# Kernel optimization log

Hardware: AMD Instinct MI355X
Metric: run time of the kernel (lower is better)

The kernel has to match this reference:

```python
import jax, jax.numpy as jnp
import numpy as np

B, N, D = 8, 4096, 1024
NC, NU = 8, 32            # core / universal experts (num_experts=16, occ_factor=1/4)
E = NC + NU               # 40 total experts
S = 2                     # slots per expert
HC, HU = 4 * D, D         # core hidden = 4*dim, occ hidden = 4*occ_factor*dim = dim
L2_EPS = 1e-6
LN_EPS = 1e-5


def l2norm(x):
    n = jnp.sqrt(jnp.sum(x * x, axis=-1, keepdims=True))
    return x * (1.0 / (n + L2_EPS))


def layernorm(x, g, b):
    mu = jnp.mean(x, axis=-1, keepdims=True)
    var = jnp.mean((x - mu) ** 2, axis=-1, keepdims=True)
    return (x - mu) / jnp.sqrt(var + LN_EPS) * g + b


def entmax15(z):
    # exact 1.5-entmax over last axis (sorted algorithm, Peters et al. 2019)
    z = z / 2.0
    z = z - jnp.max(z, axis=-1, keepdims=True)
    zs = -jnp.sort(-z, axis=-1)                      # descending
    K = z.shape[-1]
    k = jnp.arange(1, K + 1, dtype=z.dtype)
    mean = jnp.cumsum(zs, axis=-1) / k
    meansq = jnp.cumsum(zs * zs, axis=-1) / k
    ss = k * (meansq - mean * mean)
    delta = jnp.maximum((1.0 - ss) / k, 1e-12)
    tau = mean - jnp.sqrt(delta)
    support = jnp.sum((tau <= zs).astype(jnp.int32), axis=-1, keepdims=True)
    tau_star = jnp.take_along_axis(tau, support - 1, axis=-1)
    return jnp.maximum(z - tau_star, 0.0) ** 2


def setup_inputs() -> dict:
    key = jax.random.key(0)
    ks = jax.random.split(key, 8)
    return {
        "x": jax.random.normal(ks[0], (B, N, D), jnp.float32),
        "attn_weight": jax.random.uniform(ks[1], (B, 128), jnp.float32),
        "phi": jax.random.normal(ks[2], (E, S, D), jnp.float32) * 0.02,
        "key_gamma": jnp.ones((D,), jnp.float32),
        "key_beta": jnp.zeros((D,), jnp.float32),
        "query_gamma": jnp.ones((D,), jnp.float32),
        "query_beta": jnp.zeros((D,), jnp.float32),
        "ln_gamma": jnp.ones((D,), jnp.float32),
        "ln_beta": jnp.zeros((D,), jnp.float32),
        "scale0": jnp.asarray(0.5, jnp.float32),
        "scale1": jnp.asarray(0.5, jnp.float32),
        "core_w1": jax.random.normal(ks[3], (NC, D, HC), jnp.float32) * (D ** -0.5),
        "core_b1": jnp.zeros((NC, HC), jnp.float32),
        "core_w2": jax.random.normal(ks[4], (NC, HC, D), jnp.float32) * (HC ** -0.5),
        "core_b2": jnp.zeros((NC, D), jnp.float32),
        "occ_w1": jax.random.normal(ks[5], (NU, D, HU), jnp.float32) * (D ** -0.5),
        "occ_b1": jnp.zeros((NU, HU), jnp.float32),
        "occ_w2": jax.random.normal(ks[6], (NU, HU, D), jnp.float32) * (HU ** -0.5),
        "occ_b2": jnp.zeros((NU, D), jnp.float32),
    }


def _expert_mlp(s, w1, b1, w2, b2):
    # s: [b, e, s, d]; per-expert 2-layer MLP with exact GELU
    h = jax.nn.gelu(jnp.einsum('besd,edh->besh', s, w1) + b1[None, :, None, :], approximate=False)
    return jnp.einsum('besh,ehd->besd', h, w2) + b2[None, :, None, :]


def reference(x, attn_weight, phi, key_gamma, key_beta, query_gamma, query_beta,
              ln_gamma, ln_beta, scale0, scale1,
              core_w1, core_b1, core_w2, core_b2,
              occ_w1, occ_b1, occ_w2, occ_b2):
    # keys: OffsetScale then l2norm
    k = l2norm(x * key_gamma + key_beta)
    # queries: OffsetScale -> LayerNorm -> l2norm on phi
    q = layernorm(phi * query_gamma + query_beta, ln_gamma, ln_beta)
    q = l2norm(q)
    logits = jnp.einsum('bnd,esd->bnes', k, q)                      # [B,N,E,S]
    core_mask = (jnp.arange(E) < NC)[None, None, :, None]
    adjusted = jnp.where(core_mask, logits, jnp.asarray(-10000.0, logits.dtype))
    dispatch = jax.nn.softmax(adjusted / scale0, axis=2)            # softmax over experts
    combine = entmax15((adjusted / scale1).reshape(B, N, E * S))    # [B,N,E*S]
    slots = jnp.einsum('bnd,bnes->besd', x, dispatch)               # [B,E,S,D]
    core_out = _expert_mlp(slots[:, :NC], core_w1, core_b1, core_w2, core_b2)
    occ_out = _expert_mlp(slots[:, NC:], occ_w1, occ_b1, occ_w2, occ_b2)
    out = jnp.concatenate([core_out, occ_out], axis=1).reshape(B, E * S, D)
    return jnp.einsum('bsd,bns->bnd', out, combine)                 # [B,N,D]
```

## Files before the change

kernel.cpp:

```cpp
#include <hip/hip_runtime.h>
#include <hip/hip_bf16.h>

#define B_ 8
#define N_ 4096
#define D_ 1024

__global__ __launch_bounds__(64) void k_prep(
    const float* __restrict__ phi, const float* __restrict__ qg, const float* __restrict__ qb,
    const float* __restrict__ lng, const float* __restrict__ lnb,
    const float* __restrict__ kg, const float* __restrict__ kb,
    float* __restrict__ qk, float* __restrict__ cj, float* __restrict__ wbuf)
{
    int r = blockIdx.x;
    int lane = threadIdx.x;
    if (r == 16) {
        float cacc = 0.f;
#pragma unroll
        for (int c = 0; c < 16; ++c) {
            int i = c * 64 + lane;
            float g = kg[i], b = kb[i];
            wbuf[i] = g * g;
            wbuf[1024 + i] = 2.0f * g * b;
            cacc += b * b;
        }
#pragma unroll
        for (int m = 32; m; m >>= 1) cacc += __shfl_xor(cacc, m);
        if (lane == 0) wbuf[2048] = cacc;
        return;
    }
    const float* pr = phi + (size_t)r * D_;
    float v[16];
    float s1 = 0.f;
#pragma unroll
    for (int c = 0; c < 16; ++c) {
        int i = c * 64 + lane;
        v[c] = pr[i] * qg[i] + qb[i];
        s1 += v[c];
    }
#pragma unroll
    for (int m = 32; m; m >>= 1) s1 += __shfl_xor(s1, m);
    float mu = s1 * (1.0f / D_);
    float s2 = 0.f;
#pragma unroll
    for (int c = 0; c < 16; ++c) { float dd = v[c] - mu; s2 += dd * dd; }
#pragma unroll
    for (int m = 32; m; m >>= 1) s2 += __shfl_xor(s2, m);
    float var = s2 * (1.0f / D_);
    float inv = 1.0f / sqrtf(var + 1e-5f);
    float u[16];
    float s3 = 0.f;
#pragma unroll
    for (int c = 0; c < 16; ++c) {
        int i = c * 64 + lane;
        u[c] = (v[c] - mu) * inv * lng[i] + lnb[i];
        s3 += u[c] * u[c];
    }
#pragma unroll
    for (int m = 32; m; m >>= 1) s3 += __shfl_xor(s3, m);
    float rn = 1.0f / (sqrtf(s3) + 1e-6f);
    float cacc = 0.f;
#pragma unroll
    for (int c = 0; c < 16; ++c) {
        int i = c * 64 + lane;
        float qv = u[c] * rn;
        qk[(size_t)r * D_ + i] = qv * kg[i];
        cacc += qv * kb[i];
    }
#pragma unroll
    for (int m = 32; m; m >>= 1) cacc += __shfl_xor(cacc, m);
    if (lane == 0) cj[r] = cacc;
}

__global__ __launch_bounds__(256) void k_logits(
    const float* __restrict__ x, const float* __restrict__ qk,
    const float* __restrict__ wbuf, float* __restrict__ lgbuf)
{
    __shared__ float xs[2][32 * 68];
    __shared__ float qs[2][16 * 64];
    __shared__ float wsd[2][128];

    int tid = threadIdx.x;
    int tok0 = blockIdx.x * 32;
    int tok = tid & 31, gg = tid >> 5;

    float acc[17];
#pragma unroll
    for (int v = 0; v < 17; ++v) acc[v] = 0.f;

    float4 rx0, rx1, rq;
    float rw = 0.f;
    int r0 = tid >> 4, c40 = tid & 15;
    int r1 = 16 + r0;

    auto STAGE = [&](int dc) {
        rx0 = *(const float4*)(x + (size_t)(tok0 + r0) * D_ + dc * 64 + c40 * 4);
        rx1 = *(const float4*)(x + (size_t)(tok0 + r1) * D_ + dc * 64 + c40 * 4);
        rq  = *(const float4*)(qk + (size_t)(tid >> 4) * D_ + dc * 64 + (tid & 15) * 4);
        if (tid < 128) rw = wbuf[(size_t)(tid >> 6) * 1024 + dc * 64 + (tid & 63)];
    };
    auto WRITE = [&](int buf) {
        *(float4*)(&xs[buf][r0 * 68 + c40 * 4]) = rx0;
        *(float4*)(&xs[buf][r1 * 68 + c40 * 4]) = rx1;
        ((float4*)qs[buf])[tid] = rq;
        if (tid < 128) wsd[buf][tid] = rw;
    };
    auto COMPUTE = [&](int buf) {
        const float* xp = &xs[buf][tok * 68 + gg * 8];
        const float* qp = &qs[buf][gg * 8];
        const float* wp = &wsd[buf][gg * 8];
#pragma unroll
        for (int dl4 = 0; dl4 < 2; ++dl4) {
            float4 xv  = *(const float4*)(xp + dl4 * 4);
            float4 w2v = *(const float4*)(wp + dl4 * 4);
            float4 w1v = *(const float4*)(wp + 64 + dl4 * 4);
            acc[16] += (w2v.x * xv.x + w1v.x) * xv.x + (w2v.y * xv.y + w1v.y) * xv.y
                     + (w2v.z * xv.z + w1v.z) * xv.z + (w2v.w * xv.w + w1v.w) * xv.w;
#pragma unroll
            for (int j = 0; j < 16; ++j) {
                float4 q4 = *(const float4*)(qp + j * 64 + dl4 * 4);
                acc[j] += xv.x * q4.x + xv.y * q4.y + xv.z * q4.z + xv.w * q4.w;
            }
        }
    };

    STAGE(0);
    WRITE(0);
    int cur = 0;
#pragma unroll 1
    for (int dc = 0; dc < 16; ++dc) {
        if (dc < 15) STAGE(dc + 1);
        __syncthreads();
        COMPUTE(cur);
        if (dc < 15) WRITE(cur ^ 1);
        cur ^= 1;
    }
    __syncthreads();

    float* red = &xs[0][0];
#pragma unroll
    for (int v = 0; v < 17; ++v) red[(tok * 17 + v) * 8 + gg] = acc[v];
    __syncthreads();

#pragma unroll
    for (int it = 0; it < 3; ++it) {
        int idx = tid + it * 256;
        if (idx < 544) {
            float4 p0 = *(const float4*)(red + idx * 8);
            float4 p1 = *(const float4*)(red + idx * 8 + 4);
            float sum = ((p0.x + p0.y) + (p0.z + p0.w)) + ((p1.x + p1.y) + (p1.z + p1.w));
            int t = idx / 17, v = idx - t * 17;
            lgbuf[(size_t)(tok0 + t) * 20 + v] = sum;
        }
    }
}

__global__ __launch_bounds__(64) void k_epi(
    const float* __restrict__ lgbuf, const float* __restrict__ cj,
    const float* __restrict__ wbuf,
    const float* __restrict__ s0p, const float* __restrict__ s1p,
    float* __restrict__ combine, float* __restrict__ dispatch)
{
    int tok = blockIdx.x * 64 + threadIdx.x;
    const float* lp = lgbuf + (size_t)tok * 20;
    float s[17];
    float4 q0 = *(const float4*)(lp + 0);
    float4 q1 = *(const float4*)(lp + 4);
    float4 q2 = *(const float4*)(lp + 8);
    float4 q3 = *(const float4*)(lp + 12);
    s[0] = q0.x; s[1] = q0.y; s[2] = q0.z; s[3] = q0.w;
    s[4] = q1.x; s[5] = q1.y; s[6] = q1.z; s[7] = q1.w;
    s[8] = q2.x; s[9] = q2.y; s[10] = q2.z; s[11] = q2.w;
    s[12] = q3.x; s[13] = q3.y; s[14] = q3.z; s[15] = q3.w;
    s[16] = lp[16];

    float ss = s[16] + wbuf[2048];
    float rn = 1.0f / (sqrtf(ss) + 1e-6f);
    float inv0 = 1.0f / s0p[0];
    float inv1h = 0.5f / s1p[0];
    float lg[16];
#pragma unroll
    for (int j = 0; j < 16; ++j) lg[j] = (s[j] + cj[j]) * rn;

    float dsp[16];
#pragma unroll
    for (int sl = 0; sl < 2; ++sl) {
        float a[8], m = -1e30f;
#pragma unroll
        for (int ee = 0; ee < 8; ++ee) { a[ee] = lg[2 * ee + sl] * inv0; m = fmaxf(m, a[ee]); }
        float den = 0.f;
#pragma unroll
        for (int ee = 0; ee < 8; ++ee) { a[ee] = expf(a[ee] - m); den += a[ee]; }
        float r = 1.0f / den;
#pragma unroll
        for (int ee = 0; ee < 8; ++ee) dsp[2 * ee + sl] = a[ee] * r;
    }

    float z[16], zmax = -1e30f;
#pragma unroll
    for (int j = 0; j < 16; ++j) { z[j] = lg[j] * inv1h; zmax = fmaxf(zmax, z[j]); }
#pragma unroll
    for (int j = 0; j < 16; ++j) z[j] -= zmax;
    float zsr[16];
#pragma unroll
    for (int j = 0; j < 16; ++j) zsr[j] = z[j];
#pragma unroll
    for (int rr = 0; rr < 16; ++rr) {
#pragma unroll
        for (int jj = (rr & 1); jj + 1 < 16; jj += 2) {
            float aa = zsr[jj], bb = zsr[jj + 1];
            zsr[jj] = fmaxf(aa, bb);
            zsr[jj + 1] = fminf(aa, bb);
        }
    }
    float cs = 0.f, css = 0.f, tau_star = 0.f;
#pragma unroll
    for (int kk = 1; kk <= 16; ++kk) {
        cs += zsr[kk - 1];
        css += zsr[kk - 1] * zsr[kk - 1];
        float fk = (float)kk;
        float mean = cs / fk, msq = css / fk;
        float ssv = fk * (msq - mean * mean);
        float delta = fmaxf((1.0f - ssv) / fk, 1e-12f);
        float tau = mean - sqrtf(delta);
        tau_star = (tau <= zsr[kk - 1]) ? tau : tau_star;
    }
    float4* cw = (float4*)(combine + (size_t)tok * 16);
    float4* dw = (float4*)(dispatch + (size_t)tok * 16);
#pragma unroll
    for (int q4i = 0; q4i < 4; ++q4i) {
        float4 cv, dv;
        float t0 = fmaxf(z[q4i * 4 + 0] - tau_star, 0.f);
        float t1 = fmaxf(z[q4i * 4 + 1] - tau_star, 0.f);
        float t2 = fmaxf(z[q4i * 4 + 2] - tau_star, 0.f);
        float t3 = fmaxf(z[q4i * 4 + 3] - tau_star, 0.f);
        cv.x = t0 * t0; cv.y = t1 * t1; cv.z = t2 * t2; cv.w = t3 * t3;
        dv.x = dsp[q4i * 4 + 0]; dv.y = dsp[q4i * 4 + 1];
        dv.z = dsp[q4i * 4 + 2]; dv.w = dsp[q4i * 4 + 3];
        cw[q4i] = cv;
        dw[q4i] = dv;
    }
}

__global__ __launch_bounds__(256) void k_slots_partial(
    const float* __restrict__ x, const float* __restrict__ dispatch,
    float* __restrict__ partial)
{
    __shared__ float sm[2048];
    int nc = blockIdx.x, dc = blockIdx.y, b = blockIdx.z;
    int tid = threadIdx.x;
    int n0 = nc * 128;
    int d0 = dc * 512 + tid * 2;
    const float4* src = (const float4*)(dispatch + ((size_t)b * N_ + n0) * 16);
    ((float4*)sm)[tid * 2] = src[tid * 2];
    ((float4*)sm)[tid * 2 + 1] = src[tid * 2 + 1];
    __syncthreads();

    const float* xp = x + ((size_t)b * N_ + n0) * D_ + d0;
    float2 acc[16];
#pragma unroll
    for (int j = 0; j < 16; ++j) { acc[j].x = 0.f; acc[j].y = 0.f; }
#pragma unroll 4
    for (int n = 0; n < 128; ++n) {
        float2 xv = *(const float2*)(xp + (size_t)n * D_);
        const float4* q4 = (const float4*)(sm + n * 16);
        float4 s0 = q4[0], s1 = q4[1], s2 = q4[2], s3 = q4[3];
        acc[0].x  += s0.x * xv.x; acc[0].y  += s0.x * xv.y;
        acc[1].x  += s0.y * xv.x; acc[1].y  += s0.y * xv.y;
        acc[2].x  += s0.z * xv.x; acc[2].y  += s0.z * xv.y;
        acc[3].x  += s0.w * xv.x; acc[3].y  += s0.w * xv.y;
        acc[4].x  += s1.x * xv.x; acc[4].y  += s1.x * xv.y;
        acc[5].x  += s1.y * xv.x; acc[5].y  += s1.y * xv.y;
        acc[6].x  += s1.z * xv.x; acc[6].y  += s1.z * xv.y;
        acc[7].x  += s1.w * xv.x; acc[7].y  += s1.w * xv.y;
        acc[8].x  += s2.x * xv.x; acc[8].y  += s2.x * xv.y;
        acc[9].x  += s2.y * xv.x; acc[9].y  += s2.y * xv.y;
        acc[10].x += s2.z * xv.x; acc[10].y += s2.z * xv.y;
        acc[11].x += s2.w * xv.x; acc[11].y += s2.w * xv.y;
        acc[12].x += s3.x * xv.x; acc[12].y += s3.x * xv.y;
        acc[13].x += s3.y * xv.x; acc[13].y += s3.y * xv.y;
        acc[14].x += s3.z * xv.x; acc[14].y += s3.z * xv.y;
        acc[15].x += s3.w * xv.x; acc[15].y += s3.w * xv.y;
    }
    float* op = partial + (((size_t)b * 32 + nc) * 16) * 1024 + d0;
#pragma unroll
    for (int j = 0; j < 16; ++j)
        *(float2*)(op + (size_t)j * 1024) = acc[j];
}

__global__ __launch_bounds__(256) void k_slots_reduce(
    const float* __restrict__ partial, float* __restrict__ slotsT)
{
    int idx = blockIdx.x * 256 + threadIdx.x;
    int t = idx & 15;
    int k = (idx >> 4) & 1023;
    int e = idx >> 14;
    int b = t >> 1, s = t & 1;
    int j = e * 2 + s;
    const float* p = partial + ((size_t)(b * 32) * 16 + j) * 1024 + k;
    float sum = 0.f;
#pragma unroll
    for (int nc = 0; nc < 32; ++nc) sum += p[(size_t)nc * 16384];
    slotsT[idx] = sum;
}

__global__ __launch_bounds__(256) void k_mlp1(
    const float* __restrict__ w1, const float* __restrict__ slotsT,
    float* __restrict__ p1)
{
    __shared__ float sm[2048];
    int cc = blockIdx.x, ks = blockIdx.y, e = blockIdx.z;
    int tid = threadIdx.x;
    int k0 = ks * 128;
    int col = cc * 512 + tid * 2;
    const float4* src = (const float4*)(slotsT + ((size_t)e * 1024 + k0) * 16);
    ((float4*)sm)[tid * 2] = src[tid * 2];
    ((float4*)sm)[tid * 2 + 1] = src[tid * 2 + 1];
    __syncthreads();

    const float* wp = w1 + (size_t)e * 1024 * 4096 + (size_t)k0 * 4096 + col;
    float2 acc[16];
#pragma unroll
    for (int t = 0; t < 16; ++t) { acc[t].x = 0.f; acc[t].y = 0.f; }
#pragma unroll 4
    for (int kk = 0; kk < 128; ++kk) {
        float2 w = *(const float2*)(wp + (size_t)kk * 4096);
        const float4* q4 = (const float4*)(sm + kk * 16);
        float4 s0 = q4[0], s1 = q4[1], s2 = q4[2], s3 = q4[3];
        acc[0].x  += s0.x * w.x; acc[0].y  += s0.x * w.y;
        acc[1].x  += s0.y * w.x; acc[1].y  += s0.y * w.y;
        acc[2].x  += s0.z * w.x; acc[2].y  += s0.z * w.y;
        acc[3].x  += s0.w * w.x; acc[3].y  += s0.w * w.y;
        acc[4].x  += s1.x * w.x; acc[4].y  += s1.x * w.y;
        acc[5].x  += s1.y * w.x; acc[5].y  += s1.y * w.y;
        acc[6].x  += s1.z * w.x; acc[6].y  += s1.z * w.y;
        acc[7].x  += s1.w * w.x; acc[7].y  += s1.w * w.y;
        acc[8].x  += s2.x * w.x; acc[8].y  += s2.x * w.y;
        acc[9].x  += s2.y * w.x; acc[9].y  += s2.y * w.y;
        acc[10].x += s2.z * w.x; acc[10].y += s2.z * w.y;
        acc[11].x += s2.w * w.x; acc[11].y += s2.w * w.y;
        acc[12].x += s3.x * w.x; acc[12].y += s3.x * w.y;
        acc[13].x += s3.y * w.x; acc[13].y += s3.y * w.y;
        acc[14].x += s3.z * w.x; acc[14].y += s3.z * w.y;
        acc[15].x += s3.w * w.x; acc[15].y += s3.w * w.y;
    }
    float* op = p1 + (((size_t)ks * 8 + e) * 4096 + col) * 16;
#pragma unroll
    for (int q = 0; q < 4; ++q) {
        float4 a, b;
        a.x = acc[q * 4 + 0].x; a.y = acc[q * 4 + 1].x; a.z = acc[q * 4 + 2].x; a.w = acc[q * 4 + 3].x;
        b.x = acc[q * 4 + 0].y; b.y = acc[q * 4 + 1].y; b.z = acc[q * 4 + 2].y; b.w = acc[q * 4 + 3].y;
        *(float4*)(op + q * 4) = a;
        *(float4*)(op + 16 + q * 4) = b;
    }
}

__global__ __launch_bounds__(256) void k_red1(
    const float* __restrict__ p1, const float* __restrict__ b1,
    float* __restrict__ hT)
{
    int idx = blockIdx.x * 256 + threadIdx.x;
    int q = idx & 3, col = (idx >> 2) & 4095, e = idx >> 14;
    const float* p = p1 + ((size_t)e * 4096 + col) * 16 + q * 4;
    float4 s; s.x = 0.f; s.y = 0.f; s.z = 0.f; s.w = 0.f;
#pragma unroll
    for (int ks = 0; ks < 8; ++ks) {
        float4 v = *(const float4*)(p + (size_t)ks * 524288);
        s.x += v.x; s.y += v.y; s.z += v.z; s.w += v.w;
    }
    float bb = b1[(size_t)e * 4096 + col];
    s.x += bb; s.y += bb; s.z += bb; s.w += bb;
    s.x = 0.5f * s.x * (1.0f + erff(s.x * 0.70710678118654752f));
    s.y = 0.5f * s.y * (1.0f + erff(s.y * 0.70710678118654752f));
    s.z = 0.5f * s.z * (1.0f + erff(s.z * 0.70710678118654752f));
    s.w = 0.5f * s.w * (1.0f + erff(s.w * 0.70710678118654752f));
    *(float4*)(hT + ((size_t)e * 4096 + col) * 16 + q * 4) = s;
}

__global__ __launch_bounds__(256) void k_mlp2(
    const float* __restrict__ w2, const float* __restrict__ hT,
    float* __restrict__ p2)
{
    __shared__ float sm[2048];
    int cc = blockIdx.x, ks = blockIdx.y, e = blockIdx.z;
    int tid = threadIdx.x;
    int k0 = ks * 128;
    int col = cc * 512 + tid * 2;
    const float4* src = (const float4*)(hT + ((size_t)e * 4096 + k0) * 16);
    ((float4*)sm)[tid * 2] = src[tid * 2];
    ((float4*)sm)[tid * 2 + 1] = src[tid * 2 + 1];
    __syncthreads();

    const float* wp = w2 + (size_t)e * 4096 * 1024 + (size_t)k0 * 1024 + col;
    float2 acc[16];
#pragma unroll
    for (int t = 0; t < 16; ++t) { acc[t].x = 0.f; acc[t].y = 0.f; }
#pragma unroll 4
    for (int kk = 0; kk < 128; ++kk) {
        float2 w = *(const float2*)(wp + (size_t)kk * 1024);
        const float4* q4 = (const float4*)(sm + kk * 16);
        float4 s0 = q4[0], s1 = q4[1], s2 = q4[2], s3 = q4[3];
        acc[0].x  += s0.x * w.x; acc[0].y  += s0.x * w.y;
        acc[1].x  += s0.y * w.x; acc[1].y  += s0.y * w.y;
        acc[2].x  += s0.z * w.x; acc[2].y  += s0.z * w.y;
        acc[3].x  += s0.w * w.x; acc[3].y  += s0.w * w.y;
        acc[4].x  += s1.x * w.x; acc[4].y  += s1.x * w.y;
        acc[5].x  += s1.y * w.x; acc[5].y  += s1.y * w.y;
        acc[6].x  += s1.z * w.x; acc[6].y  += s1.z * w.y;
        acc[7].x  += s1.w * w.x; acc[7].y  += s1.w * w.y;
        acc[8].x  += s2.x * w.x; acc[8].y  += s2.x * w.y;
        acc[9].x  += s2.y * w.x; acc[9].y  += s2.y * w.y;
        acc[10].x += s2.z * w.x; acc[10].y += s2.z * w.y;
        acc[11].x += s2.w * w.x; acc[11].y += s2.w * w.y;
        acc[12].x += s3.x * w.x; acc[12].y += s3.x * w.y;
        acc[13].x += s3.y * w.x; acc[13].y += s3.y * w.y;
        acc[14].x += s3.z * w.x; acc[14].y += s3.z * w.y;
        acc[15].x += s3.w * w.x; acc[15].y += s3.w * w.y;
    }
    float* op = p2 + (((size_t)ks * 8 + e) * 1024 + col) * 16;
#pragma unroll
    for (int q = 0; q < 4; ++q) {
        float4 a, b;
        a.x = acc[q * 4 + 0].x; a.y = acc[q * 4 + 1].x; a.z = acc[q * 4 + 2].x; a.w = acc[q * 4 + 3].x;
        b.x = acc[q * 4 + 0].y; b.y = acc[q * 4 + 1].y; b.z = acc[q * 4 + 2].y; b.w = acc[q * 4 + 3].y;
        *(float4*)(op + q * 4) = a;
        *(float4*)(op + 16 + q * 4) = b;
    }
}

__global__ __launch_bounds__(256) void k_red2(
    const float* __restrict__ p2, const float* __restrict__ b2,
    float* __restrict__ co)
{
    int idx = blockIdx.x * 256 + threadIdx.x;
    if (idx >= 8192) return;
    int d = idx & 1023, e = idx >> 10;
    const float* p = p2 + ((size_t)e * 1024 + d) * 16;
    float4 a0, a1, a2, a3;
    a0.x=a0.y=a0.z=a0.w=0.f; a1.x=a1.y=a1.z=a1.w=0.f;
    a2.x=a2.y=a2.z=a2.w=0.f; a3.x=a3.y=a3.z=a3.w=0.f;
#pragma unroll
    for (int ks = 0; ks < 32; ++ks) {
        const float4* v = (const float4*)(p + (size_t)ks * 131072);
        float4 v0 = v[0], v1 = v[1], v2 = v[2], v3 = v[3];
        a0.x += v0.x; a0.y += v0.y; a0.z += v0.z; a0.w += v0.w;
        a1.x += v1.x; a1.y += v1.y; a1.z += v1.z; a1.w += v1.w;
        a2.x += v2.x; a2.y += v2.y; a2.z += v2.z; a2.w += v2.w;
        a3.x += v3.x; a3.y += v3.y; a3.z += v3.z; a3.w += v3.w;
    }
    float bb = b2[(size_t)e * 1024 + d];
    float vv[16] = { a0.x, a0.y, a0.z, a0.w, a1.x, a1.y, a1.z, a1.w,
                     a2.x, a2.y, a2.z, a2.w, a3.x, a3.y, a3.z, a3.w };
#pragma unroll
    for (int t = 0; t < 16; ++t) {
        int b = t >> 1, s = t & 1;
        co[((size_t)b * 16 + e * 2 + s) * 1024 + d] = vv[t] + bb;
    }
}

__global__ __launch_bounds__(256) void k_out(
    const float* __restrict__ co, const float* __restrict__ combine,
    float* __restrict__ out)
{
    int b = blockIdx.y, tile = blockIdx.x;
    int tid = threadIdx.x;
    float4 cv[16];
#pragma unroll
    for (int j = 0; j < 16; ++j)
        cv[j] = ((const float4*)(co + ((size_t)b * 16 + j) * 1024))[tid];
    const float* cb = combine + ((size_t)b * N_ + tile * 64) * 16;
    float4* ob = (float4*)(out + ((size_t)b * N_ + tile * 64) * 1024) + tid;
    for (int it = 0; it < 64; ++it) {
        const float* cm = cb + it * 16;
        float4 acc; acc.x = 0.f; acc.y = 0.f; acc.z = 0.f; acc.w = 0.f;
#pragma unroll
        for (int j = 0; j < 16; ++j) {
            float wj = cm[j];
            acc.x += wj * cv[j].x; acc.y += wj * cv[j].y;
            acc.z += wj * cv[j].z; acc.w += wj * cv[j].w;
        }
        ob[(size_t)it * 256] = acc;
    }
}

extern "C" void kernel_launch(void* const* d_in, const int* in_sizes, int n_in,
                              void* d_out, int out_size, void* d_ws, size_t ws_size,
                              hipStream_t stream)
{
    const float* x   = (const float*)d_in[0];
    const float* phi = (const float*)d_in[2];
    const float* kg  = (const float*)d_in[3];
    const float* kb  = (const float*)d_in[4];
    const float* qg  = (const float*)d_in[5];
    const float* qb  = (const float*)d_in[6];
    const float* lng = (const float*)d_in[7];
    const float* lnb = (const float*)d_in[8];
    const float* s0  = (const float*)d_in[9];
    const float* s1  = (const float*)d_in[10];
    const float* w1  = (const float*)d_in[11];
    const float* b1  = (const float*)d_in[12];
    const float* w2  = (const float*)d_in[13];
    const float* b2  = (const float*)d_in[14];

    float* out = (float*)d_out;
    float* ws  = (float*)d_ws;

    float* qk       = ws;
    float* cj       = qk + 16384;
    float* wbuf     = cj + 16;
    float* combine  = wbuf + 2064;
    float* dispatch = combine + 524288;
    float* slotsT   = dispatch + 524288;
    float* hT       = slotsT + 131072;
    float* co       = hT + 524288;
    float* arena    = co + 131072;
    float* lgbuf    = arena;
    float* spart    = arena;
    float* p1       = arena;
    float* p2       = arena;

    k_prep         <<<dim3(17),         dim3(64),  0, stream>>>(phi, qg, qb, lng, lnb, kg, kb, qk, cj, wbuf);
    k_logits       <<<dim3(1024),       dim3(256), 0, stream>>>(x, qk, wbuf, lgbuf);
    k_epi          <<<dim3(512),        dim3(64),  0, stream>>>(lgbuf, cj, wbuf, s0, s1, combine, dispatch);
    k_slots_partial<<<dim3(32, 2, 8),   dim3(256), 0, stream>>>(x, dispatch, spart);
    k_slots_reduce <<<dim3(512),        dim3(256), 0, stream>>>(spart, slotsT);
    k_mlp1         <<<dim3(8, 8, 8),    dim3(256), 0, stream>>>(w1, slotsT, p1);
    k_red1         <<<dim3(512),        dim3(256), 0, stream>>>(p1, b1, hT);
    k_mlp2         <<<dim3(2, 32, 8),   dim3(256), 0, stream>>>(w2, hT, p2);
    k_red2         <<<dim3(32),         dim3(256), 0, stream>>>(p2, b2, co);
    k_out          <<<dim3(64, 8),      dim3(256), 0, stream>>>(co, combine, out);
}
```

Measured before the change: 246.6 us.

## Retile logits, slots and expert MLP kernels for wider per-thread work

Each k_logits block now computes 64 tokens instead of 32, so the staged q vectors are reused across two token sets. The slots and both MLP GEMV-style kernels switch from float2 to float4 columns per thread and use shorter K chunks, which gives more split-K partials and different grids. The slots and second-layer reductions are restructured to match, and k_out stages the combine weights in shared memory. The aim is better register reuse and wider memory accesses, at the cost of more partial-sum traffic and higher register pressure.

```diff
diff --git a/kernel.cpp b/kernel.cpp
--- a/kernel.cpp
+++ b/kernel.cpp
@@ -75,50 +75,56 @@
     const float* __restrict__ x, const float* __restrict__ qk,
     const float* __restrict__ wbuf, float* __restrict__ lgbuf)
 {
-    __shared__ float xs[2][32 * 68];
+    __shared__ float xs[2][64 * 68];
     __shared__ float qs[2][16 * 64];
     __shared__ float wsd[2][128];
 
     int tid = threadIdx.x;
-    int tok0 = blockIdx.x * 32;
-    int tok = tid & 31, gg = tid >> 5;
-
-    float acc[17];
-#pragma unroll
-    for (int v = 0; v < 17; ++v) acc[v] = 0.f;
-
-    float4 rx0, rx1, rq;
+    int tok0 = blockIdx.x * 64;
+    int tok32 = tid & 31, gg = tid >> 5;
+    int sr = tid >> 4, sc = tid & 15;
+
+    float accA[17], accB[17];
+#pragma unroll
+    for (int v = 0; v < 17; ++v) { accA[v] = 0.f; accB[v] = 0.f; }
+
+    float4 rx[4], rq;
     float rw = 0.f;
-    int r0 = tid >> 4, c40 = tid & 15;
-    int r1 = 16 + r0;
 
     auto STAGE = [&](int dc) {
-        rx0 = *(const float4*)(x + (size_t)(tok0 + r0) * D_ + dc * 64 + c40 * 4);
-        rx1 = *(const float4*)(x + (size_t)(tok0 + r1) * D_ + dc * 64 + c40 * 4);
-        rq  = *(const float4*)(qk + (size_t)(tid >> 4) * D_ + dc * 64 + (tid & 15) * 4);
+#pragma unroll
+        for (int i = 0; i < 4; ++i)
+            rx[i] = *(const float4*)(x + (size_t)(tok0 + sr + 16 * i) * D_ + dc * 64 + sc * 4);
+        rq = *(const float4*)(qk + (size_t)sr * D_ + dc * 64 + sc * 4);
         if (tid < 128) rw = wbuf[(size_t)(tid >> 6) * 1024 + dc * 64 + (tid & 63)];
     };
     auto WRITE = [&](int buf) {
-        *(float4*)(&xs[buf][r0 * 68 + c40 * 4]) = rx0;
-        *(float4*)(&xs[buf][r1 * 68 + c40 * 4]) = rx1;
+#pragma unroll
+        for (int i = 0; i < 4; ++i)
+            *(float4*)(&xs[buf][(sr + 16 * i) * 68 + sc * 4]) = rx[i];
         ((float4*)qs[buf])[tid] = rq;
         if (tid < 128) wsd[buf][tid] = rw;
     };
     auto COMPUTE = [&](int buf) {
-        const float* xp = &xs[buf][tok * 68 + gg * 8];
+        const float* xpA = &xs[buf][tok32 * 68 + gg * 8];
+        const float* xpB = &xs[buf][(32 + tok32) * 68 + gg * 8];
         const float* qp = &qs[buf][gg * 8];
         const float* wp = &wsd[buf][gg * 8];
 #pragma unroll
         for (int dl4 = 0; dl4 < 2; ++dl4) {
-            float4 xv  = *(const float4*)(xp + dl4 * 4);
+            float4 xvA = *(const float4*)(xpA + dl4 * 4);
+            float4 xvB = *(const float4*)(xpB + dl4 * 4);
             float4 w2v = *(const float4*)(wp + dl4 * 4);
             float4 w1v = *(const float4*)(wp + 64 + dl4 * 4);
-            acc[16] += (w2v.x * xv.x + w1v.x) * xv.x + (w2v.y * xv.y + w1v.y) * xv.y
-                     + (w2v.z * xv.z + w1v.z) * xv.z + (w2v.w * xv.w + w1v.w) * xv.w;
+            accA[16] += (w2v.x * xvA.x + w1v.x) * xvA.x + (w2v.y * xvA.y + w1v.y) * xvA.y
+                      + (w2v.z * xvA.z + w1v.z) * xvA.z + (w2v.w * xvA.w + w1v.w) * xvA.w;
+            accB[16] += (w2v.x * xvB.x + w1v.x) * xvB.x + (w2v.y * xvB.y + w1v.y) * xvB.y
+                      + (w2v.z * xvB.z + w1v.z) * xvB.z + (w2v.w * xvB.w + w1v.w) * xvB.w;
 #pragma unroll
             for (int j = 0; j < 16; ++j) {
                 float4 q4 = *(const float4*)(qp + j * 64 + dl4 * 4);
-                acc[j] += xv.x * q4.x + xv.y * q4.y + xv.z * q4.z + xv.w * q4.w;
+                accA[j] += xvA.x * q4.x + xvA.y * q4.y + xvA.z * q4.z + xvA.w * q4.w;
+                accB[j] += xvB.x * q4.x + xvB.y * q4.y + xvB.z * q4.z + xvB.w * q4.w;
             }
         }
     };
@@ -138,13 +144,16 @@
 
     float* red = &xs[0][0];
 #pragma unroll
-    for (int v = 0; v < 17; ++v) red[(tok * 17 + v) * 8 + gg] = acc[v];
+    for (int v = 0; v < 17; ++v) {
+        red[(tok32 * 17 + v) * 8 + gg] = accA[v];
+        red[((32 + tok32) * 17 + v) * 8 + gg] = accB[v];
+    }
     __syncthreads();
 
 #pragma unroll
-    for (int it = 0; it < 3; ++it) {
+    for (int it = 0; it < 5; ++it) {
         int idx = tid + it * 256;
-        if (idx < 544) {
+        if (idx < 1088) {
             float4 p0 = *(const float4*)(red + idx * 8);
             float4 p1 = *(const float4*)(red + idx * 8 + 4);
             float sum = ((p0.x + p0.y) + (p0.z + p0.w)) + ((p1.x + p1.y) + (p1.z + p1.w));
@@ -245,112 +254,111 @@
     const float* __restrict__ x, const float* __restrict__ dispatch,
     float* __restrict__ partial)
 {
-    __shared__ float sm[2048];
-    int nc = blockIdx.x, dc = blockIdx.y, b = blockIdx.z;
+    __shared__ float sm[1024];
+    int nc = blockIdx.x, b = blockIdx.y;
     int tid = threadIdx.x;
-    int n0 = nc * 128;
-    int d0 = dc * 512 + tid * 2;
-    const float4* src = (const float4*)(dispatch + ((size_t)b * N_ + n0) * 16);
-    ((float4*)sm)[tid * 2] = src[tid * 2];
-    ((float4*)sm)[tid * 2 + 1] = src[tid * 2 + 1];
+    int n0 = nc * 64;
+    ((float4*)sm)[tid] = ((const float4*)(dispatch + ((size_t)b * N_ + n0) * 16))[tid];
     __syncthreads();
 
-    const float* xp = x + ((size_t)b * N_ + n0) * D_ + d0;
-    float2 acc[16];
-#pragma unroll
-    for (int j = 0; j < 16; ++j) { acc[j].x = 0.f; acc[j].y = 0.f; }
-#pragma unroll 4
-    for (int n = 0; n < 128; ++n) {
-        float2 xv = *(const float2*)(xp + (size_t)n * D_);
+    const float* xp = x + ((size_t)b * N_ + n0) * D_ + tid * 4;
+    float4 acc[16];
+#pragma unroll
+    for (int j = 0; j < 16; ++j) { acc[j].x = 0.f; acc[j].y = 0.f; acc[j].z = 0.f; acc[j].w = 0.f; }
+#pragma unroll 8
+    for (int n = 0; n < 64; ++n) {
+        float4 xv = *(const float4*)(xp + (size_t)n * D_);
         const float4* q4 = (const float4*)(sm + n * 16);
         float4 s0 = q4[0], s1 = q4[1], s2 = q4[2], s3 = q4[3];
-        acc[0].x  += s0.x * xv.x; acc[0].y  += s0.x * xv.y;
-        acc[1].x  += s0.y * xv.x; acc[1].y  += s0.y * xv.y;
-        acc[2].x  += s0.z * xv.x; acc[2].y  += s0.z * xv.y;
-        acc[3].x  += s0.w * xv.x; acc[3].y  += s0.w * xv.y;
-        acc[4].x  += s1.x * xv.x; acc[4].y  += s1.x * xv.y;
-        acc[5].x  += s1.y * xv.x; acc[5].y  += s1.y * xv.y;
-        acc[6].x  += s1.z * xv.x; acc[6].y  += s1.z * xv.y;
-        acc[7].x  += s1.w * xv.x; acc[7].y  += s1.w * xv.y;
-        acc[8].x  += s2.x * xv.x; acc[8].y  += s2.x * xv.y;
-        acc[9].x  += s2.y * xv.x; acc[9].y  += s2.y * xv.y;
-        acc[10].x += s2.z * xv.x; acc[10].y += s2.z * xv.y;
-        acc[11].x += s2.w * xv.x; acc[11].y += s2.w * xv.y;
-        acc[12].x += s3.x * xv.x; acc[12].y += s3.x * xv.y;
-        acc[13].x += s3.y * xv.x; acc[13].y += s3.y * xv.y;
-        acc[14].x += s3.z * xv.x; acc[14].y += s3.z * xv.y;
-        acc[15].x += s3.w * xv.x; acc[15].y += s3.w * xv.y;
-    }
-    float* op = partial + (((size_t)b * 32 + nc) * 16) * 1024 + d0;
+        acc[0].x  += s0.x * xv.x; acc[0].y  += s0.x * xv.y; acc[0].z  += s0.x * xv.z; acc[0].w  += s0.x * xv.w;
+        acc[1].x  += s0.y * xv.x; acc[1].y  += s0.y * xv.y; acc[1].z  += s0.y * xv.z; acc[1].w  += s0.y * xv.w;
+        acc[2].x  += s0.z * xv.x; acc[2].y  += s0.z * xv.y; acc[2].z  += s0.z * xv.z; acc[2].w  += s0.z * xv.w;
+        acc[3].x  += s0.w * xv.x; acc[3].y  += s0.w * xv.y; acc[3].z  += s0.w * xv.z; acc[3].w  += s0.w * xv.w;
+        acc[4].x  += s1.x * xv.x; acc[4].y  += s1.x * xv.y; acc[4].z  += s1.x * xv.z; acc[4].w  += s1.x * xv.w;
+        acc[5].x  += s1.y * xv.x; acc[5].y  += s1.y * xv.y; acc[5].z  += s1.y * xv.z; acc[5].w  += s1.y * xv.w;
+        acc[6].x  += s1.z * xv.x; acc[6].y  += s1.z * xv.y; acc[6].z  += s1.z * xv.z; acc[6].w  += s1.z * xv.w;
+        acc[7].x  += s1.w * xv.x; acc[7].y  += s1.w * xv.y; acc[7].z  += s1.w * xv.z; acc[7].w  += s1.w * xv.w;
+        acc[8].x  += s2.x * xv.x; acc[8].y  += s2.x * xv.y; acc[8].z  += s2.x * xv.z; acc[8].w  += s2.x * xv.w;
+        acc[9].x  += s2.y * xv.x; acc[9].y  += s2.y * xv.y; acc[9].z  += s2.y * xv.z; acc[9].w  += s2.y * xv.w;
+        acc[10].x += s2.z * xv.x; acc[10].y += s2.z * xv.y; acc[10].z += s2.z * xv.z; acc[10].w += s2.z * xv.w;
+        acc[11].x += s2.w * xv.x; acc[11].y += s2.w * xv.y; acc[11].z += s2.w * xv.z; acc[11].w += s2.w * xv.w;
+        acc[12].x += s3.x * xv.x; acc[12].y += s3.x * xv.y; acc[12].z += s3.x * xv.z; acc[12].w += s3.x * xv.w;
+        acc[13].x += s3.y * xv.x; acc[13].y += s3.y * xv.y; acc[13].z += s3.y * xv.z; acc[13].w += s3.y * xv.w;
+        acc[14].x += s3.z * xv.x; acc[14].y += s3.z * xv.y; acc[14].z += s3.z * xv.z; acc[14].w += s3.z * xv.w;
+        acc[15].x += s3.w * xv.x; acc[15].y += s3.w * xv.y; acc[15].z += s3.w * xv.z; acc[15].w += s3.w * xv.w;
+    }
+    float* op = partial + (((size_t)b * 64 + nc) * 16) * 1024 + tid * 4;
 #pragma unroll
     for (int j = 0; j < 16; ++j)
-        *(float2*)(op + (size_t)j * 1024) = acc[j];
+        *(float4*)(op + (size_t)j * 1024) = acc[j];
 }
 
 __global__ __launch_bounds__(256) void k_slots_reduce(
     const float* __restrict__ partial, float* __restrict__ slotsT)
 {
-    int idx = blockIdx.x * 256 + threadIdx.x;
-    int t = idx & 15;
-    int k = (idx >> 4) & 1023;
-    int e = idx >> 14;
-    int b = t >> 1, s = t & 1;
-    int j = e * 2 + s;
-    const float* p = partial + ((size_t)(b * 32) * 16 + j) * 1024 + k;
-    float sum = 0.f;
-#pragma unroll
-    for (int nc = 0; nc < 32; ++nc) sum += p[(size_t)nc * 16384];
-    slotsT[idx] = sum;
+    int j = blockIdx.x, b = blockIdx.y;
+    int tid = threadIdx.x;
+    const float* p = partial + ((size_t)(b * 64) * 16 + j) * 1024 + tid * 4;
+    float4 s; s.x = 0.f; s.y = 0.f; s.z = 0.f; s.w = 0.f;
+#pragma unroll 8
+    for (int nc = 0; nc < 64; ++nc) {
+        float4 v = *(const float4*)(p + (size_t)nc * 16384);
+        s.x += v.x; s.y += v.y; s.z += v.z; s.w += v.w;
+    }
+    int e = j >> 1, sl = j & 1;
+    int t = b * 2 + sl;
+    float* o = slotsT + ((size_t)e * 1024 + tid * 4) * 16 + t;
+    o[0] = s.x; o[16] = s.y; o[32] = s.z; o[48] = s.w;
 }
 
 __global__ __launch_bounds__(256) void k_mlp1(
     const float* __restrict__ w1, const float* __restrict__ slotsT,
     float* __restrict__ p1)
 {
-    __shared__ float sm[2048];
+    __shared__ float sm[1024];
     int cc = blockIdx.x, ks = blockIdx.y, e = blockIdx.z;
     int tid = threadIdx.x;
-    int k0 = ks * 128;
-    int col = cc * 512 + tid * 2;
-    const float4* src = (const float4*)(slotsT + ((size_t)e * 1024 + k0) * 16);
-    ((float4*)sm)[tid * 2] = src[tid * 2];
-    ((float4*)sm)[tid * 2 + 1] = src[tid * 2 + 1];
+    int k0 = ks * 64;
+    int col = cc * 1024 + tid * 4;
+    ((float4*)sm)[tid] = ((const float4*)(slotsT + ((size_t)e * 1024 + k0) * 16))[tid];
     __syncthreads();
 
     const float* wp = w1 + (size_t)e * 1024 * 4096 + (size_t)k0 * 4096 + col;
-    float2 acc[16];
-#pragma unroll
-    for (int t = 0; t < 16; ++t) { acc[t].x = 0.f; acc[t].y = 0.f; }
-#pragma unroll 4
-    for (int kk = 0; kk < 128; ++kk) {
-        float2 w = *(const float2*)(wp + (size_t)kk * 4096);
+    float4 acc[16];
+#pragma unroll
+    for (int t = 0; t < 16; ++t) { acc[t].x = 0.f; acc[t].y = 0.f; acc[t].z = 0.f; acc[t].w = 0.f; }
+#pragma unroll 8
+    for (int kk = 0; kk < 64; ++kk) {
+        float4 w = *(const float4*)(wp + (size_t)kk * 4096);
         const float4* q4 = (const float4*)(sm + kk * 16);
         float4 s0 = q4[0], s1 = q4[1], s2 = q4[2], s3 = q4[3];
-        acc[0].x  += s0.x * w.x; acc[0].y  += s0.x * w.y;
-        acc[1].x  += s0.y * w.x; acc[1].y  += s0.y * w.y;
-        acc[2].x  += s0.z * w.x; acc[2].y  += s0.z * w.y;
-        acc[3].x  += s0.w * w.x; acc[3].y  += s0.w * w.y;
-        acc[4].x  += s1.x * w.x; acc[4].y  += s1.x * w.y;
-        acc[5].x  += s1.y * w.x; acc[5].y  += s1.y * w.y;
-        acc[6].x  += s1.z * w.x; acc[6].y  += s1.z * w.y;
-        acc[7].x  += s1.w * w.x; acc[7].y  += s1.w * w.y;
-        acc[8].x  += s2.x * w.x; acc[8].y  += s2.x * w.y;
-        acc[9].x  += s2.y * w.x; acc[9].y  += s2.y * w.y;
-        acc[10].x += s2.z * w.x; acc[10].y += s2.z * w.y;
-        acc[11].x += s2.w * w.x; acc[11].y += s2.w * w.y;
-        acc[12].x += s3.x * w.x; acc[12].y += s3.x * w.y;
-        acc[13].x += s3.y * w.x; acc[13].y += s3.y * w.y;
-        acc[14].x += s3.z * w.x; acc[14].y += s3.z * w.y;
-        acc[15].x += s3.w * w.x; acc[15].y += s3.w * w.y;
-    }
+        acc[0].x  += s0.x * w.x; acc[0].y  += s0.x * w.y; acc[0].z  += s0.x * w.z; acc[0].w  += s0.x * w.w;
+        acc[1].x  += s0.y * w.x; acc[1].y  += s0.y * w.y; acc[1].z  += s0.y * w.z; acc[1].w  += s0.y * w.w;
+        acc[2].x  += s0.z * w.x; acc[2].y  += s0.z * w.y; acc[2].z  += s0.z * w.z; acc[2].w  += s0.z * w.w;
+        acc[3].x  += s0.w * w.x; acc[3].y  += s0.w * w.y; acc[3].z  += s0.w * w.z; acc[3].w  += s0.w * w.w;
+        acc[4].x  += s1.x * w.x; acc[4].y  += s1.x * w.y; acc[4].z  += s1.x * w.z; acc[4].w  += s1.x * w.w;
+        acc[5].x  += s1.y * w.x; acc[5].y  += s1.y * w.y; acc[5].z  += s1.y * w.z; acc[5].w  += s1.y * w.w;
+        acc[6].x  += s1.z * w.x; acc[6].y  += s1.z * w.y; acc[6].z  += s1.z * w.z; acc[6].w  += s1.z * w.w;
+        acc[7].x  += s1.w * w.x; acc[7].y  += s1.w * w.y; acc[7].z  += s1.w * w.z; acc[7].w  += s1.w * w.w;
+        acc[8].x  += s2.x * w.x; acc[8].y  += s2.x * w.y; acc[8].z  += s2.x * w.z; acc[8].w  += s2.x * w.w;
+        acc[9].x  += s2.y * w.x; acc[9].y  += s2.y * w.y; acc[9].z  += s2.y * w.z; acc[9].w  += s2.y * w.w;
+        acc[10].x += s2.z * w.x; acc[10].y += s2.z * w.y; acc[10].z += s2.z * w.z; acc[10].w += s2.z * w.w;
+        acc[11].x += s2.w * w.x; acc[11].y += s2.w * w.y; acc[11].z += s2.w * w.z; acc[11].w += s2.w * w.w;
+        acc[12].x += s3.x * w.x; acc[12].y += s3.x * w.y; acc[12].z += s3.x * w.z; acc[12].w += s3.x * w.w;
+        acc[13].x += s3.y * w.x; acc[13].y += s3.y * w.y; acc[13].z += s3.y * w.z; acc[13].w += s3.y * w.w;
+        acc[14].x += s3.z * w.x; acc[14].y += s3.z * w.y; acc[14].z += s3.z * w.z; acc[14].w += s3.z * w.w;
+        acc[15].x += s3.w * w.x; acc[15].y += s3.w * w.y; acc[15].z += s3.w * w.z; acc[15].w += s3.w * w.w;
+    }
+    float av0[16], av1[16], av2[16], av3[16];
+#pragma unroll
+    for (int t = 0; t < 16; ++t) { av0[t] = acc[t].x; av1[t] = acc[t].y; av2[t] = acc[t].z; av3[t] = acc[t].w; }
     float* op = p1 + (((size_t)ks * 8 + e) * 4096 + col) * 16;
 #pragma unroll
     for (int q = 0; q < 4; ++q) {
-        float4 a, b;
-        a.x = acc[q * 4 + 0].x; a.y = acc[q * 4 + 1].x; a.z = acc[q * 4 + 2].x; a.w = acc[q * 4 + 3].x;
-        b.x = acc[q * 4 + 0].y; b.y = acc[q * 4 + 1].y; b.z = acc[q * 4 + 2].y; b.w = acc[q * 4 + 3].y;
-        *(float4*)(op + q * 4) = a;
-        *(float4*)(op + 16 + q * 4) = b;
+        *(float4*)(op + 0 * 16 + q * 4) = make_float4(av0[q*4+0], av0[q*4+1], av0[q*4+2], av0[q*4+3]);
+        *(float4*)(op + 1 * 16 + q * 4) = make_float4(av1[q*4+0], av1[q*4+1], av1[q*4+2], av1[q*4+3]);
+        *(float4*)(op + 2 * 16 + q * 4) = make_float4(av2[q*4+0], av2[q*4+1], av2[q*4+2], av2[q*4+3]);
+        *(float4*)(op + 3 * 16 + q * 4) = make_float4(av3[q*4+0], av3[q*4+1], av3[q*4+2], av3[q*4+3]);
     }
 }
 
@@ -363,7 +371,7 @@
     const float* p = p1 + ((size_t)e * 4096 + col) * 16 + q * 4;
     float4 s; s.x = 0.f; s.y = 0.f; s.z = 0.f; s.w = 0.f;
 #pragma unroll
-    for (int ks = 0; ks < 8; ++ks) {
+    for (int ks = 0; ks < 16; ++ks) {
         float4 v = *(const float4*)(p + (size_t)ks * 524288);
         s.x += v.x; s.y += v.y; s.z += v.z; s.w += v.w;
     }
@@ -380,50 +388,50 @@
     const float* __restrict__ w2, const float* __restrict__ hT,
     float* __restrict__ p2)
 {
-    __shared__ float sm[2048];
-    int cc = blockIdx.x, ks = blockIdx.y, e = blockIdx.z;
+    __shared__ float sm[1024];
+    int ks = blockIdx.x, e = blockIdx.y;
     int tid = threadIdx.x;
-    int k0 = ks * 128;
-    int col = cc * 512 + tid * 2;
-    const float4* src = (const float4*)(hT + ((size_t)e * 4096 + k0) * 16);
-    ((float4*)sm)[tid * 2] = src[tid * 2];
-    ((float4*)sm)[tid * 2 + 1] = src[tid * 2 + 1];
+    int k0 = ks * 64;
+    int col = tid * 4;
+    ((float4*)sm)[tid] = ((const float4*)(hT + ((size_t)e * 4096 + k0) * 16))[tid];
     __syncthreads();
 
     const float* wp = w2 + (size_t)e * 4096 * 1024 + (size_t)k0 * 1024 + col;
-    float2 acc[16];
-#pragma unroll
-    for (int t = 0; t < 16; ++t) { acc[t].x = 0.f; acc[t].y = 0.f; }
-#pragma unroll 4
-    for (int kk = 0; kk < 128; ++kk) {
-        float2 w = *(const float2*)(wp + (size_t)kk * 1024);
+    float4 acc[16];
+#pragma unroll
+    for (int t = 0; t < 16; ++t) { acc[t].x = 0.f; acc[t].y = 0.f; acc[t].z = 0.f; acc[t].w = 0.f; }
+#pragma unroll 8
+    for (int kk = 0; kk < 64; ++kk) {
+        float4 w = *(const float4*)(wp + (size_t)kk * 1024);
         const float4* q4 = (const float4*)(sm + kk * 16);
         float4 s0 = q4[0], s1 = q4[1], s2 = q4[2], s3 = q4[3];
-        acc[0].x  += s0.x * w.x; acc[0].y  += s0.x * w.y;
-        acc[1].x  += s0.y * w.x; acc[1].y  += s0.y * w.y;
-        acc[2].x  += s0.z * w.x; acc[2].y  += s0.z * w.y;
-        acc[3].x  += s0.w * w.x; acc[3].y  += s0.w * w.y;
-        acc[4].x  += s1.x * w.x; acc[4].y  += s1.x * w.y;
-        acc[5].x  += s1.y * w.x; acc[5].y  += s1.y * w.y;
-        acc[6].x  += s1.z * w.x; acc[6].y  += s1.z * w.y;
-        acc[7].x  += s1.w * w.x; acc[7].y  += s1.w * w.y;
-        acc[8].x  += s2.x * w.x; acc[8].y  += s2.x * w.y;
-        acc[9].x  += s2.y * w.x; acc[9].y  += s2.y * w.y;
-        acc[10].x += s2.z * w.x; acc[10].y += s2.z * w.y;
-        acc[11].x += s2.w * w.x; acc[11].y += s2.w * w.y;
-        acc[12].x += s3.x * w.x; acc[12].y += s3.x * w.y;
-        acc[13].x += s3.y * w.x; acc[13].y += s3.y * w.y;
-        acc[14].x += s3.z * w.x; acc[14].y += s3.z * w.y;
-        acc[15].x += s3.w * w.x; acc[15].y += s3.w * w.y;
-    }
+        acc[0].x  += s0.x * w.x; acc[0].y  += s0.x * w.y; acc[0].z  += s0.x * w.z; acc[0].w  += s0.x * w.w;
+        acc[1].x  += s0.y * w.x; acc[1].y  += s0.y * w.y; acc[1].z  += s0.y * w.z; acc[1].w  += s0.y * w.w;
+        acc[2].x  += s0.z * w.x; acc[2].y  += s0.z * w.y; acc[2].z  += s0.z * w.z; acc[2].w  += s0.z * w.w;
+        acc[3].x  += s0.w * w.x; acc[3].y  += s0.w * w.y; acc[3].z  += s0.w * w.z; acc[3].w  += s0.w * w.w;
+        acc[4].x  += s1.x * w.x; acc[4].y  += s1.x * w.y; acc[4].z  += s1.x * w.z; acc[4].w  += s1.x * w.w;
+        acc[5].x  += s1.y * w.x; acc[5].y  += s1.y * w.y; acc[5].z  += s1.y * w.z; acc[5].w  += s1.y * w.w;
+        acc[6].x  += s1.z * w.x; acc[6].y  += s1.z * w.y; acc[6].z  += s1.z * w.z; acc[6].w  += s1.z * w.w;
+        acc[7].x  += s1.w * w.x; acc[7].y  += s1.w * w.y; acc[7].z  += s1.w * w.z; acc[7].w  += s1.w * w.w;
+        acc[8].x  += s2.x * w.x; acc[8].y  += s2.x * w.y; acc[8].z  += s2.x * w.z; acc[8].w  += s2.x * w.w;
+        acc[9].x  += s2.y * w.x; acc[9].y  += s2.y * w.y; acc[9].z  += s2.y * w.z; acc[9].w  += s2.y * w.w;
+        acc[10].x += s2.z * w.x; acc[10].y += s2.z * w.y; acc[10].z += s2.z * w.z; acc[10].w += s2.z * w.w;
+        acc[11].x += s2.w * w.x; acc[11].y += s2.w * w.y; acc[11].z += s2.w * w.z; acc[11].w += s2.w * w.w;
+        acc[12].x += s3.x * w.x; acc[12].y += s3.x * w.y; acc[12].z += s3.x * w.z; acc[12].w += s3.x * w.w;
+        acc[13].x += s3.y * w.x; acc[13].y += s3.y * w.y; acc[13].z += s3.y * w.z; acc[13].w += s3.y * w.w;
+        acc[14].x += s3.z * w.x; acc[14].y += s3.z * w.y; acc[14].z += s3.z * w.z; acc[14].w += s3.z * w.w;
+        acc[15].x += s3.w * w.x; acc[15].y += s3.w * w.y; acc[15].z += s3.w * w.z; acc[15].w += s3.w * w.w;
+    }
+    float av0[16], av1[16], av2[16], av3[16];
+#pragma unroll
+    for (int t = 0; t < 16; ++t) { av0[t] = acc[t].x; av1[t] = acc[t].y; av2[t] = acc[t].z; av3[t] = acc[t].w; }
     float* op = p2 + (((size_t)ks * 8 + e) * 1024 + col) * 16;
 #pragma unroll
     for (int q = 0; q < 4; ++q) {
-        float4 a, b;
-        a.x = acc[q * 4 + 0].x; a.y = acc[q * 4 + 1].x; a.z = acc[q * 4 + 2].x; a.w = acc[q * 4 + 3].x;
-        b.x = acc[q * 4 + 0].y; b.y = acc[q * 4 + 1].y; b.z = acc[q * 4 + 2].y; b.w = acc[q * 4 + 3].y;
-        *(float4*)(op + q * 4) = a;
-        *(float4*)(op + 16 + q * 4) = b;
+        *(float4*)(op + 0 * 16 + q * 4) = make_float4(av0[q*4+0], av0[q*4+1], av0[q*4+2], av0[q*4+3]);
+        *(float4*)(op + 1 * 16 + q * 4) = make_float4(av1[q*4+0], av1[q*4+1], av1[q*4+2], av1[q*4+3]);
+        *(float4*)(op + 2 * 16 + q * 4) = make_float4(av2[q*4+0], av2[q*4+1], av2[q*4+2], av2[q*4+3]);
+        *(float4*)(op + 3 * 16 + q * 4) = make_float4(av3[q*4+0], av3[q*4+1], av3[q*4+2], av3[q*4+3]);
     }
 }
 
@@ -432,28 +440,21 @@
     float* __restrict__ co)
 {
     int idx = blockIdx.x * 256 + threadIdx.x;
-    if (idx >= 8192) return;
-    int d = idx & 1023, e = idx >> 10;
-    const float* p = p2 + ((size_t)e * 1024 + d) * 16;
-    float4 a0, a1, a2, a3;
-    a0.x=a0.y=a0.z=a0.w=0.f; a1.x=a1.y=a1.z=a1.w=0.f;
-    a2.x=a2.y=a2.z=a2.w=0.f; a3.x=a3.y=a3.z=a3.w=0.f;
-#pragma unroll
-    for (int ks = 0; ks < 32; ++ks) {
-        const float4* v = (const float4*)(p + (size_t)ks * 131072);
-        float4 v0 = v[0], v1 = v[1], v2 = v[2], v3 = v[3];
-        a0.x += v0.x; a0.y += v0.y; a0.z += v0.z; a0.w += v0.w;
-        a1.x += v1.x; a1.y += v1.y; a1.z += v1.z; a1.w += v1.w;
-        a2.x += v2.x; a2.y += v2.y; a2.z += v2.z; a2.w += v2.w;
-        a3.x += v3.x; a3.y += v3.y; a3.z += v3.z; a3.w += v3.w;
+    int q = idx & 3, d = (idx >> 2) & 1023, e = idx >> 12;
+    const float* p = p2 + ((size_t)e * 1024 + d) * 16 + q * 4;
+    float4 s; s.x = 0.f; s.y = 0.f; s.z = 0.f; s.w = 0.f;
+#pragma unroll 8
+    for (int ks = 0; ks < 64; ++ks) {
+        float4 v = *(const float4*)(p + (size_t)ks * 131072);
+        s.x += v.x; s.y += v.y; s.z += v.z; s.w += v.w;
     }
     float bb = b2[(size_t)e * 1024 + d];
-    float vv[16] = { a0.x, a0.y, a0.z, a0.w, a1.x, a1.y, a1.z, a1.w,
-                     a2.x, a2.y, a2.z, a2.w, a3.x, a3.y, a3.z, a3.w };
-#pragma unroll
-    for (int t = 0; t < 16; ++t) {
-        int b = t >> 1, s = t & 1;
-        co[((size_t)b * 16 + e * 2 + s) * 1024 + d] = vv[t] + bb;
+    float vv[4] = { s.x + bb, s.y + bb, s.z + bb, s.w + bb };
+#pragma unroll
+    for (int u = 0; u < 4; ++u) {
+        int t = q * 4 + u;
+        int b = t >> 1, sl = t & 1;
+        co[((size_t)b * 16 + e * 2 + sl) * 1024 + d] = vv[u];
     }
 }
 
@@ -461,16 +462,19 @@
     const float* __restrict__ co, const float* __restrict__ combine,
     float* __restrict__ out)
 {
+    __shared__ float sm[1024];
     int b = blockIdx.y, tile = blockIdx.x;
     int tid = threadIdx.x;
+    ((float4*)sm)[tid] = ((const float4*)(combine + ((size_t)b * N_ + tile * 64) * 16))[tid];
     float4 cv[16];
 #pragma unroll
     for (int j = 0; j < 16; ++j)
         cv[j] = ((const float4*)(co + ((size_t)b * 16 + j) * 1024))[tid];
-    const float* cb = combine + ((size_t)b * N_ + tile * 64) * 16;
+    __syncthreads();
     float4* ob = (float4*)(out + ((size_t)b * N_ + tile * 64) * 1024) + tid;
+#pragma unroll 2
     for (int it = 0; it < 64; ++it) {
-        const float* cm = cb + it * 16;
+        const float* cm = sm + it * 16;
         float4 acc; acc.x = 0.f; acc.y = 0.f; acc.z = 0.f; acc.w = 0.f;
 #pragma unroll
         for (int j = 0; j < 16; ++j) {
@@ -518,14 +522,14 @@
     float* p1       = arena;
     float* p2       = arena;
 
-    k_prep         <<<dim3(17),         dim3(64),  0, stream>>>(phi, qg, qb, lng, lnb, kg, kb, qk, cj, wbuf);
-    k_logits       <<<dim3(1024),       dim3(256), 0, stream>>>(x, qk, wbuf, lgbuf);
-    k_epi          <<<dim3(512),        dim3(64),  0, stream>>>(lgbuf, cj, wbuf, s0, s1, combine, dispatch);
-    k_slots_partial<<<dim3(32, 2, 8),   dim3(256), 0, stream>>>(x, dispatch, spart);
-    k_slots_reduce <<<dim3(512),        dim3(256), 0, stream>>>(spart, slotsT);
-    k_mlp1         <<<dim3(8, 8, 8),    dim3(256), 0, stream>>>(w1, slotsT, p1);
-    k_red1         <<<dim3(512),        dim3(256), 0, stream>>>(p1, b1, hT);
-    k_mlp2         <<<dim3(2, 32, 8),   dim3(256), 0, stream>>>(w2, hT, p2);
-    k_red2         <<<dim3(32),         dim3(256), 0, stream>>>(p2, b2, co);
-    k_out          <<<dim3(64, 8),      dim3(256), 0, stream>>>(co, combine, out);
-}
+    k_prep         <<<dim3(17),        dim3(64),  0, stream>>>(phi, qg, qb, lng, lnb, kg, kb, qk, cj, wbuf);
+    k_logits       <<<dim3(512),       dim3(256), 0, stream>>>(x, qk, wbuf, lgbuf);
+    k_epi          <<<dim3(512),       dim3(64),  0, stream>>>(lgbuf, cj, wbuf, s0, s1, combine, dispatch);
+    k_slots_partial<<<dim3(64, 8),     dim3(256), 0, stream>>>(x, dispatch, spart);
+    k_slots_reduce <<<dim3(16, 8),     dim3(256), 0, stream>>>(spart, slotsT);
+    k_mlp1         <<<dim3(4, 16, 8),  dim3(256), 0, stream>>>(w1, slotsT, p1);
+    k_red1         <<<dim3(512),       dim3(256), 0, stream>>>(p1, b1, hT);
+    k_mlp2         <<<dim3(64, 8),     dim3(256), 0, stream>>>(w2, hT, p2);
+    k_red2         <<<dim3(128),       dim3(256), 0, stream>>>(p2, b2, co);
+    k_out          <<<dim3(64, 8),     dim3(256), 0, stream>>>(co, combine, out);
+}
```

Measured after the change: 248.9 us. No clear change (+0.9%).
